# Optimization experiments

Hardware: AMD Instinct MI355X
Metric: run time of the kernel (lower is better)

Reference implementation:

```python
import jax, jax.numpy as jnp
import numpy as np

B, H, S, D = 2, 12, 2048, 128
SCALE = D ** (-0.5)
LAMBDA_INIT = 0.8


def setup_inputs() -> dict:
    key = jax.random.key(0)
    ks = jax.random.split(key, 5)
    shp = (B, H, S, D)
    return {
        "q1": jax.random.normal(ks[0], shp, dtype=jnp.float32),
        "k1": jax.random.normal(ks[1], shp, dtype=jnp.float32),
        "v": jax.random.normal(ks[2], shp, dtype=jnp.float32),
        "q2": jax.random.normal(ks[3], shp, dtype=jnp.float32),
        "k2": jax.random.normal(ks[4], shp, dtype=jnp.float32),
        # learnable lambda parameter, stored in log space (lambda_init=0.8)
        "lambda_log": jnp.full((1,), np.log(LAMBDA_INIT), dtype=jnp.float32),
    }


def _causal_attn(q, k, v, causal_mask):
    # q,k,v: [B,H,S,D]; causal_mask: [S,S] bool (True = keep)
    scores = jnp.einsum("bhqd,bhkd->bhqk", q, k) * SCALE
    neg = jnp.asarray(jnp.finfo(scores.dtype).min, scores.dtype)
    scores = jnp.where(causal_mask, scores, neg)
    weights = jax.nn.softmax(scores, axis=-1)
    return jnp.einsum("bhqk,bhkd->bhqd", weights, v)


def reference(q1, k1, v, q2, k2, lambda_log):
    seq = q1.shape[2]
    causal_mask = jnp.tril(jnp.ones((seq, seq), dtype=bool))
    attn1 = _causal_attn(q1, k1, v, causal_mask)
    attn2 = _causal_attn(q2, k2, v, causal_mask)
    lambda_val = jnp.exp(lambda_log).astype(q1.dtype)  # scalar-shaped (1,)
    return attn1 - lambda_val * attn2
```

## Files before the change

### kernel.cpp

```cpp
#include <hip/hip_runtime.h>

#define S_LEN 2048
#define D_DIM 128
#define NBH   24
#define TELEM (NBH * S_LEN * D_DIM)
#define SC2  (0.08838834764831845f * 1.44269504088896f)
#define MFIX 20.0f

typedef __bf16 bf16x8 __attribute__((ext_vector_type(8)));
typedef float f32x4 __attribute__((ext_vector_type(4)));
union Frag { bf16x8 v; unsigned short h[8]; uint4 q; };

#define PSTR 40
#define BUFU 12288
#define SMEM_USH (2 * BUFU)

__device__ __forceinline__ unsigned short f2bf(float f) {
    union { float f; unsigned u; } x; x.f = f;
    unsigned r = x.u + 0x7fffu + ((x.u >> 16) & 1u);
    return (unsigned short)(r >> 16);
}
__device__ __forceinline__ unsigned pk2bf(float a, float b) {
    return (unsigned)f2bf(a) | ((unsigned)f2bf(b) << 16);
}

typedef __attribute__((address_space(1))) const unsigned int gu32;
typedef __attribute__((address_space(3))) unsigned int lu32;
__device__ __forceinline__ void g2l16(const unsigned short* g, unsigned short* l) {
    __builtin_amdgcn_global_load_lds((gu32*)g, (lu32*)l, 16, 0, 0);
}

#define KBLK (TELEM / (8 * 256))
__global__ __launch_bounds__(256) void conv_kv(
    const float* __restrict__ gk1, const float* __restrict__ gk2, const float* __restrict__ gv,
    unsigned short* __restrict__ ok1, unsigned short* __restrict__ ok2,
    unsigned short* __restrict__ ovt)
{
    __shared__ __align__(16) unsigned short sT[128 * 40];
    const int b = blockIdx.x;
    if (b < 2 * KBLK) {
        const float* src = (b < KBLK) ? gk1 : gk2;
        unsigned short* dst = (b < KBLK) ? ok1 : ok2;
        const int bb = (b < KBLK) ? b : b - KBLK;
        const size_t base = ((size_t)bb * 256 + threadIdx.x) * 8;
        float4 a = *(const float4*)(src + base);
        float4 c = *(const float4*)(src + base + 4);
        uint4 w = {pk2bf(a.x, a.y), pk2bf(a.z, a.w), pk2bf(c.x, c.y), pk2bf(c.z, c.w)};
        *(uint4*)(dst + base) = w;
        return;
    }
    const int bx  = b - 2 * KBLK;
    const int tid  = threadIdx.x;
    const int wave = tid >> 6;
    const int lane = tid & 63;
    const int quad = lane >> 4;
    const int l16  = lane & 15;
    const int bh = bx >> 6;
    const int s0 = (bx & 63) * 32;
    const float* pv = gv + (size_t)bh * S_LEN * D_DIM + (size_t)s0 * D_DIM;
    const int vd0 = (wave >> 1) * 64 + l16 * 4;
    const int pq  = ((quad & 1) << 1) | (quad >> 1);
    #pragma unroll
    for (int i = 0; i < 4; ++i) {
        const int kvb = i * 8 + (wave & 1) * 4;
        float4 f = *(const float4*)(pv + (kvb + quad) * D_DIM + vd0);
        unsigned h01 = pk2bf(f.x, f.y), h23 = pk2bf(f.z, f.w);
        unsigned t01 = (unsigned)__shfl_xor((int)h01, 16);
        unsigned t23 = (unsigned)__shfl_xor((int)h23, 16);
        unsigned b01, b23;
        if (quad & 1) {
            b01 = (t23 & 0xffffu) | (h23 << 16);
            b23 = (t23 >> 16) | (h23 & 0xffff0000u);
        } else {
            b01 = (h01 & 0xffffu) | (t01 << 16);
            b23 = (h01 >> 16) | (t01 & 0xffff0000u);
        }
        unsigned s01 = (unsigned)__shfl_xor((int)b01, 32);
        unsigned s23 = (unsigned)__shfl_xor((int)b23, 32);
        uint2 w;
        if (quad & 2) { w.x = s23; w.y = b23; }
        else          { w.x = b01; w.y = s01; }
        *(uint2*)&sT[(vd0 + pq) * 40 + kvb] = w;
    }
    __syncthreads();
    const int d = tid >> 1;
    const int h = tid & 1;
    uint4 w0 = *(const uint4*)&sT[d * 40 + h * 16];
    uint4 w1 = *(const uint4*)&sT[d * 40 + h * 16 + 8];
    unsigned short* out = ovt + ((size_t)bh * D_DIM + d) * S_LEN + s0 + h * 16;
    *(uint4*)(out) = w0;
    *(uint4*)(out + 8) = w1;
}

__device__ __forceinline__ void stage_tile(
    unsigned short* smem, int boff, int w,
    const int* koff, const int* voff,
    const unsigned short* k1pl, const unsigned short* k2pl, const unsigned short* vpl,
    int kv0)
{
    const unsigned short* kp1 = k1pl + (size_t)kv0 * 128;
    const unsigned short* kp2 = k2pl + (size_t)kv0 * 128;
    const unsigned short* vp  = vpl + kv0;
    unsigned short* dk1 = smem + boff + w * 1024;
    unsigned short* dk2 = smem + boff + 4096 + w * 1024;
    unsigned short* dv  = smem + boff + 8192 + w * 1024;
    #pragma unroll
    for (int j = 0; j < 2; ++j) {
        g2l16(kp1 + koff[j], dk1 + j * 512);
        g2l16(kp2 + koff[j], dk2 + j * 512);
        g2l16(vp  + voff[j], dv  + j * 512);
    }
}

__global__ __launch_bounds__(256, 3) void diff_attn_fast(
    const float* __restrict__ gq1, const float* __restrict__ gq2,
    const float* __restrict__ gll,
    const unsigned short* __restrict__ k1b, const unsigned short* __restrict__ k2b,
    const unsigned short* __restrict__ vtb, float* __restrict__ gout)
{
    __shared__ __align__(16) unsigned short smem[SMEM_USH];

    const int tid  = threadIdx.x;
    const int w    = tid >> 6;
    const int lane = tid & 63;
    const int quad = lane >> 4;
    const int l16  = lane & 15;
    const int g    = w & 1;

    const int bid   = blockIdx.x;
    const int j     = bid / NBH;
    const int bh    = bid - j * NBH;
    const int i     = 31 - j;
    const int T     = 2 * i + 2;
    const int sidx  = (w < 2) ? (2 * i + 1) : (2 * i);
    const int qw    = sidx * 32;
    const int mytiles = sidx + 1;
    const size_t hoff = (size_t)bh * (S_LEN * D_DIM);

    const float lam = __expf(gll[0]);

    Frag q1f[4], q2f[4];
    {
        const float* p1 = gq1 + hoff + (size_t)(qw + g * 16 + l16) * D_DIM;
        const float* p2 = gq2 + hoff + (size_t)(qw + g * 16 + l16) * D_DIM;
        #pragma unroll
        for (int ks = 0; ks < 4; ++ks) {
            const int d0 = ks * 32 + quad * 8;
            float4 a = *(const float4*)(p1 + d0);
            float4 b = *(const float4*)(p1 + d0 + 4);
            q1f[ks].q = (uint4){pk2bf(a.x, a.y), pk2bf(a.z, a.w),
                                pk2bf(b.x, b.y), pk2bf(b.z, b.w)};
            a = *(const float4*)(p2 + d0);
            b = *(const float4*)(p2 + d0 + 4);
            q2f[ks].q = (uint4){pk2bf(a.x, a.y), pk2bf(a.z, a.w),
                                pk2bf(b.x, b.y), pk2bf(b.z, b.w)};
        }
    }

    int koff[2], voff[2];
    #pragma unroll
    for (int jj = 0; jj < 2; ++jj) {
        const int s = w * 8 + jj * 4 + quad;
        koff[jj] = s * 128 + ((l16 ^ (s & 15)) << 3);
        const int d = w * 32 + jj * 16 + (lane >> 2);
        voff[jj] = d * 2048 + (((lane & 3) ^ ((d >> 1) & 3)) << 3);
    }
    const unsigned short* k1pl = k1b + hoff;
    const unsigned short* k2pl = k2b + hoff;
    const unsigned short* vpl  = vtb + hoff;

    f32x4 o1[8], o2[8];
    #pragma unroll
    for (int ii = 0; ii < 8; ++ii) {
        o1[ii] = (f32x4){0.f, 0.f, 0.f, 0.f};
        o2[ii] = (f32x4){0.f, 0.f, 0.f, 0.f};
    }
    float l1a = 0.f, l2a = 0.f;

    __asm__ __volatile__("s_waitcnt vmcnt(0)" ::: "memory");
    stage_tile(smem, 0, w, koff, voff, k1pl, k2pl, vpl, 0);

    int boff = 0;
    for (int t = 0; t < T; ++t) {
        const int nboff = boff ^ BUFU;
        __asm__ __volatile__("s_waitcnt vmcnt(0) lgkmcnt(0)" ::: "memory");
        __builtin_amdgcn_s_barrier();
        __asm__ __volatile__("" ::: "memory");
        if (t + 1 < T)
            stage_tile(smem, nboff, w, koff, voff, k1pl, k2pl, vpl, (t + 1) * 32);

        if (t < mytiles) {
            const unsigned short* sK1 = smem + boff;
            const unsigned short* sK2 = smem + boff + 4096;
            const unsigned short* sVt = smem + boff + 8192;
            const int kv0 = t * 32;

            f32x4 sA[2], sB[2];
            #pragma unroll
            for (int sub = 0; sub < 2; ++sub) {
                sA[sub] = (f32x4){0.f, 0.f, 0.f, 0.f};
                sB[sub] = (f32x4){0.f, 0.f, 0.f, 0.f};
            }
            __builtin_amdgcn_s_setprio(1);
            #pragma unroll
            for (int sub = 0; sub < 2; ++sub) {
                const int srow = (sub * 16 + l16) * 128;
                #pragma unroll
                for (int ks = 0; ks < 4; ++ks) {
                    const int c = ks * 4 + quad;
                    Frag kf;
                    kf.q = *(const uint4*)&sK1[srow + ((c ^ l16) << 3)];
                    sA[sub] = __builtin_amdgcn_mfma_f32_16x16x32_bf16(kf.v, q1f[ks].v, sA[sub], 0, 0, 0);
                    kf.q = *(const uint4*)&sK2[srow + ((c ^ l16) << 3)];
                    sB[sub] = __builtin_amdgcn_mfma_f32_16x16x32_bf16(kf.v, q2f[ks].v, sB[sub], 0, 0, 0);
                }
            }
            __builtin_amdgcn_s_setprio(0);

            const bool full = (t < sidx);
            float p1v[8], p2v[8];
            if (full) {
                #pragma unroll
                for (int sub = 0; sub < 2; ++sub)
                    #pragma unroll
                    for (int r = 0; r < 4; ++r) {
                        p1v[sub * 4 + r] = __builtin_amdgcn_exp2f(sA[sub][r] * SC2 - MFIX);
                        p2v[sub * 4 + r] = __builtin_amdgcn_exp2f(sB[sub][r] * SC2 - MFIX);
                    }
            } else {
                const int qv = qw + g * 16 + l16;
                #pragma unroll
                for (int sub = 0; sub < 2; ++sub)
                    #pragma unroll
                    for (int r = 0; r < 4; ++r) {
                        const int kv = kv0 + sub * 16 + quad * 4 + r;
                        const bool ok = (kv <= qv);
                        p1v[sub * 4 + r] = __builtin_amdgcn_exp2f(ok ? sA[sub][r] * SC2 - MFIX : -1e30f);
                        p2v[sub * 4 + r] = __builtin_amdgcn_exp2f(ok ? sB[sub][r] * SC2 - MFIX : -1e30f);
                    }
            }
            float a1 = 0.f, a2 = 0.f;
            #pragma unroll
            for (int ii = 0; ii < 8; ++ii) { a1 += p1v[ii]; a2 += p2v[ii]; }
            l1a += a1; l2a += a2;

            Frag pf1, pf2;
            {
                unsigned a0 = pk2bf(p1v[0], p1v[1]);
                unsigned a1w = pk2bf(p1v[2], p1v[3]);
                unsigned a2 = pk2bf(p1v[4], p1v[5]);
                unsigned a3 = pk2bf(p1v[6], p1v[7]);
                asm("v_permlane32_swap_b32 %0, %1" : "+v"(a0), "+v"(a2));
                asm("v_permlane32_swap_b32 %0, %1" : "+v"(a1w), "+v"(a3));
                asm("v_permlane16_swap_b32 %0, %1" : "+v"(a0), "+v"(a2));
                asm("v_permlane16_swap_b32 %0, %1" : "+v"(a1w), "+v"(a3));
                pf1.q = (uint4){a0, a1w, a2, a3};
                unsigned b0 = pk2bf(p2v[0], p2v[1]);
                unsigned b1w = pk2bf(p2v[2], p2v[3]);
                unsigned b2 = pk2bf(p2v[4], p2v[5]);
                unsigned b3 = pk2bf(p2v[6], p2v[7]);
                asm("v_permlane32_swap_b32 %0, %1" : "+v"(b0), "+v"(b2));
                asm("v_permlane32_swap_b32 %0, %1" : "+v"(b1w), "+v"(b3));
                asm("v_permlane16_swap_b32 %0, %1" : "+v"(b0), "+v"(b2));
                asm("v_permlane16_swap_b32 %0, %1" : "+v"(b1w), "+v"(b3));
                pf2.q = (uint4){b0, b1w, b2, b3};
            }

            __builtin_amdgcn_s_setprio(1);
            #pragma unroll
            for (int cb = 0; cb < 8; ++cb) {
                const int d = cb * 16 + l16;
                Frag vf;
                vf.q = *(const uint4*)&sVt[d * 32 + ((quad ^ ((d >> 1) & 3)) << 3)];
                o1[cb] = __builtin_amdgcn_mfma_f32_16x16x32_bf16(vf.v, pf1.v, o1[cb], 0, 0, 0);
                o2[cb] = __builtin_amdgcn_mfma_f32_16x16x32_bf16(vf.v, pf2.v, o2[cb], 0, 0, 0);
            }
            __builtin_amdgcn_s_setprio(0);
        }
        boff = nboff;
    }

    __asm__ __volatile__("s_waitcnt lgkmcnt(0)" ::: "memory");
    __builtin_amdgcn_s_barrier();
    __asm__ __volatile__("" ::: "memory");

    float l1 = l1a, l2 = l2a;
    l1 += __shfl_xor(l1, 16); l1 += __shfl_xor(l1, 32);
    l2 += __shfl_xor(l2, 16); l2 += __shfl_xor(l2, 32);
    const float inv1 = 1.0f / l1;
    const float inv2 = lam / l2;
    float* sO = (float*)smem + w * 2112;
    #pragma unroll
    for (int cb = 0; cb < 8; ++cb) {
        f32x4 r = o1[cb] * inv1 - o2[cb] * inv2;
        *(f32x4*)&sO[l16 * 132 + cb * 16 + quad * 4] = r;
    }
    __asm__ __volatile__("s_waitcnt lgkmcnt(0)" ::: "memory");
    #pragma unroll
    for (int u = 0; u < 8; ++u) {
        const int row = u * 2 + (lane >> 5);
        const int d4  = lane & 31;
        f32x4 vv = *(const f32x4*)&sO[row * 132 + d4 * 4];
        *(f32x4*)(gout + hoff + (size_t)(qw + g * 16 + row) * D_DIM + d4 * 4) = vv;
    }
}

#define KSTR 136
#define VSTR2 40
#define foK1 0
#define foK2 (32 * KSTR)
#define foVt (2 * 32 * KSTR)
#define foP  (2 * 32 * KSTR + 128 * VSTR2)
#define FSMEM (foP + 4 * 2 * 16 * PSTR)

__global__ __launch_bounds__(256) void diff_attn_slow(
    const float* __restrict__ gq1, const float* __restrict__ gk1,
    const float* __restrict__ gv,  const float* __restrict__ gq2,
    const float* __restrict__ gk2, const float* __restrict__ gll,
    float* __restrict__ gout)
{
    __shared__ __align__(16) unsigned short smem[FSMEM];
    unsigned short* sK1 = smem + foK1;
    unsigned short* sK2 = smem + foK2;
    unsigned short* sVt = smem + foVt;

    const int tid  = threadIdx.x;
    const int wave = tid >> 6;
    const int lane = tid & 63;
    const int quad = lane >> 4;
    const int l16  = lane & 15;
    const int qb   = (int)gridDim.x - 1 - (int)blockIdx.x;
    const int bh   = blockIdx.y;
    const size_t hoff = (size_t)bh * S_LEN * D_DIM;
    const int qbase = qb * 64 + wave * 16;

    unsigned short* sP1 = smem + foP + (wave * 2 + 0) * 16 * PSTR;
    unsigned short* sP2 = smem + foP + (wave * 2 + 1) * 16 * PSTR;

    const float lam = __expf(gll[0]);

    Frag q1f[4], q2f[4];
    {
        const float* p1 = gq1 + hoff + (size_t)(qbase + l16) * D_DIM;
        const float* p2 = gq2 + hoff + (size_t)(qbase + l16) * D_DIM;
        #pragma unroll
        for (int ks = 0; ks < 4; ++ks) {
            const int d0 = ks * 32 + quad * 8;
            float4 a = *(const float4*)(p1 + d0);
            float4 b = *(const float4*)(p1 + d0 + 4);
            q1f[ks].q = (uint4){pk2bf(a.x, a.y), pk2bf(a.z, a.w),
                               pk2bf(b.x, b.y), pk2bf(b.z, b.w)};
            a = *(const float4*)(p2 + d0);
            b = *(const float4*)(p2 + d0 + 4);
            q2f[ks].q = (uint4){pk2bf(a.x, a.y), pk2bf(a.z, a.w),
                               pk2bf(b.x, b.y), pk2bf(b.z, b.w)};
        }
    }

    f32x4 o1[8], o2[8];
    #pragma unroll
    for (int i = 0; i < 8; ++i) {
        o1[i] = (f32x4){0.f, 0.f, 0.f, 0.f};
        o2[i] = (f32x4){0.f, 0.f, 0.f, 0.f};
    }
    float m1 = -1e30f, m2 = -1e30f, l1 = 0.f, l2 = 0.f;

    const int ntiles  = qb * 2 + 2;
    const int mytiles = (qbase + 15) / 32 + 1;

    const int vd0 = (wave >> 1) * 64 + l16 * 4;
    const int pq  = ((quad & 1) << 1) | (quad >> 1);

    for (int t = 0; t < ntiles; ++t) {
        __syncthreads();
        const int kv0 = t * 32;
        {
            const float* pk1 = gk1 + hoff + (size_t)kv0 * D_DIM;
            const float* pk2 = gk2 + hoff + (size_t)kv0 * D_DIM;
            #pragma unroll
            for (int i = 0; i < 4; ++i) {
                const int e   = i * 256 + tid;
                const int row = e >> 5;
                const int c4  = e & 31;
                const int go  = row * D_DIM + c4 * 4;
                float4 f = *(const float4*)(pk1 + go);
                uint2 w; w.x = pk2bf(f.x, f.y); w.y = pk2bf(f.z, f.w);
                *(uint2*)&sK1[row * KSTR + c4 * 4] = w;
                f = *(const float4*)(pk2 + go);
                w.x = pk2bf(f.x, f.y); w.y = pk2bf(f.z, f.w);
                *(uint2*)&sK2[row * KSTR + c4 * 4] = w;
            }
        }
        {
            const float* pv = gv + hoff + (size_t)kv0 * D_DIM;
            #pragma unroll
            for (int i = 0; i < 4; ++i) {
                const int kvb = i * 8 + (wave & 1) * 4;
                float4 f = *(const float4*)(pv + (kvb + quad) * D_DIM + vd0);
                unsigned h01 = pk2bf(f.x, f.y), h23 = pk2bf(f.z, f.w);
                unsigned t01 = (unsigned)__shfl_xor((int)h01, 16);
                unsigned t23 = (unsigned)__shfl_xor((int)h23, 16);
                unsigned b01, b23;
                if (quad & 1) {
                    b01 = (t23 & 0xffffu) | (h23 << 16);
                    b23 = (t23 >> 16) | (h23 & 0xffff0000u);
                } else {
                    b01 = (h01 & 0xffffu) | (t01 << 16);
                    b23 = (h01 >> 16) | (t01 & 0xffff0000u);
                }
                unsigned s01 = (unsigned)__shfl_xor((int)b01, 32);
                unsigned s23 = (unsigned)__shfl_xor((int)b23, 32);
                uint2 w;
                if (quad & 2) { w.x = s23; w.y = b23; }
                else          { w.x = b01; w.y = s01; }
                *(uint2*)&sVt[(vd0 + pq) * VSTR2 + kvb] = w;
            }
        }
        __syncthreads();
        if (t >= mytiles) continue;

        f32x4 s1[2], s2[2];
        #pragma unroll
        for (int sub = 0; sub < 2; ++sub) {
            s1[sub] = (f32x4){0.f, 0.f, 0.f, 0.f};
            s2[sub] = (f32x4){0.f, 0.f, 0.f, 0.f};
            const int ro = (sub * 16 + l16) * KSTR + quad * 8;
            #pragma unroll
            for (int ks = 0; ks < 4; ++ks) {
                Frag kf;
                kf.q = *(const uint4*)&sK1[ro + ks * 32];
                s1[sub] = __builtin_amdgcn_mfma_f32_16x16x32_bf16(kf.v, q1f[ks].v, s1[sub], 0, 0, 0);
                kf.q = *(const uint4*)&sK2[ro + ks * 32];
                s2[sub] = __builtin_amdgcn_mfma_f32_16x16x32_bf16(kf.v, q2f[ks].v, s2[sub], 0, 0, 0);
            }
        }

        const int qv = qbase + l16;
        {
            float a[8];
            #pragma unroll
            for (int sub = 0; sub < 2; ++sub)
                #pragma unroll
                for (int r = 0; r < 4; ++r) {
                    const int kv = kv0 + sub * 16 + quad * 4 + r;
                    a[sub * 4 + r] = (kv <= qv) ? s1[sub][r] * SC2 : -__builtin_inff();
                }
            float mt = a[0];
            #pragma unroll
            for (int i = 1; i < 8; ++i) mt = fmaxf(mt, a[i]);
            mt = fmaxf(mt, __shfl_xor(mt, 16));
            mt = fmaxf(mt, __shfl_xor(mt, 32));
            const float mn = fmaxf(m1, mt);
            const float al = __builtin_amdgcn_exp2f(m1 - mn);
            m1 = mn;
            float p[8], rs = 0.f;
            #pragma unroll
            for (int i = 0; i < 8; ++i) { p[i] = __builtin_amdgcn_exp2f(a[i] - mn); rs += p[i]; }
            rs += __shfl_xor(rs, 16);
            rs += __shfl_xor(rs, 32);
            l1 = l1 * al + rs;
            #pragma unroll
            for (int cb = 0; cb < 8; ++cb) o1[cb] *= al;
            uint2 w;
            w.x = pk2bf(p[0], p[1]); w.y = pk2bf(p[2], p[3]);
            *(uint2*)&sP1[l16 * PSTR + quad * 4] = w;
            w.x = pk2bf(p[4], p[5]); w.y = pk2bf(p[6], p[7]);
            *(uint2*)&sP1[l16 * PSTR + 16 + quad * 4] = w;
        }
        {
            float a[8];
            #pragma unroll
            for (int sub = 0; sub < 2; ++sub)
                #pragma unroll
                for (int r = 0; r < 4; ++r) {
                    const int kv = kv0 + sub * 16 + quad * 4 + r;
                    a[sub * 4 + r] = (kv <= qv) ? s2[sub][r] * SC2 : -__builtin_inff();
                }
            float mt = a[0];
            #pragma unroll
            for (int i = 1; i < 8; ++i) mt = fmaxf(mt, a[i]);
            mt = fmaxf(mt, __shfl_xor(mt, 16));
            mt = fmaxf(mt, __shfl_xor(mt, 32));
            const float mn = fmaxf(m2, mt);
            const float al = __builtin_amdgcn_exp2f(m2 - mn);
            m2 = mn;
            float p[8], rs = 0.f;
            #pragma unroll
            for (int i = 0; i < 8; ++i) { p[i] = __builtin_amdgcn_exp2f(a[i] - mn); rs += p[i]; }
            rs += __shfl_xor(rs, 16);
            rs += __shfl_xor(rs, 32);
            l2 = l2 * al + rs;
            #pragma unroll
            for (int cb = 0; cb < 8; ++cb) o2[cb] *= al;
            uint2 w;
            w.x = pk2bf(p[0], p[1]); w.y = pk2bf(p[2], p[3]);
            *(uint2*)&sP2[l16 * PSTR + quad * 4] = w;
            w.x = pk2bf(p[4], p[5]); w.y = pk2bf(p[6], p[7]);
            *(uint2*)&sP2[l16 * PSTR + 16 + quad * 4] = w;
        }

        __asm__ __volatile__("s_waitcnt lgkmcnt(0)" ::: "memory");

        Frag pf1, pf2;
        pf1.q = *(const uint4*)&sP1[l16 * PSTR + quad * 8];
        pf2.q = *(const uint4*)&sP2[l16 * PSTR + quad * 8];
        #pragma unroll
        for (int cb = 0; cb < 8; ++cb) {
            Frag vf;
            vf.q = *(const uint4*)&sVt[(cb * 16 + l16) * VSTR2 + quad * 8];
            o1[cb] = __builtin_amdgcn_mfma_f32_16x16x32_bf16(vf.v, pf1.v, o1[cb], 0, 0, 0);
            o2[cb] = __builtin_amdgcn_mfma_f32_16x16x32_bf16(vf.v, pf2.v, o2[cb], 0, 0, 0);
        }
    }

    __syncthreads();
    float* sO = (float*)smem + wave * (16 * 132);
    const float inv1 = 1.0f / l1;
    const float inv2 = lam / l2;
    #pragma unroll
    for (int cb = 0; cb < 8; ++cb) {
        f32x4 r = o1[cb] * inv1 - o2[cb] * inv2;
        *(f32x4*)&sO[l16 * 132 + cb * 16 + quad * 4] = r;
    }
    __asm__ __volatile__("s_waitcnt lgkmcnt(0)" ::: "memory");
    #pragma unroll
    for (int u = 0; u < 8; ++u) {
        const int row = u * 2 + (lane >> 5);
        const int d4  = lane & 31;
        f32x4 vv = *(const f32x4*)&sO[row * 132 + d4 * 4];
        *(f32x4*)(gout + hoff + (size_t)(qbase + row) * D_DIM + d4 * 4) = vv;
    }
}

extern "C" void kernel_launch(void* const* d_in, const int* in_sizes, int n_in,
                              void* d_out, int out_size, void* d_ws, size_t ws_size,
                              hipStream_t stream) {
    (void)in_sizes; (void)n_in; (void)out_size;
    const float* gq1 = (const float*)d_in[0];
    const float* gk1 = (const float*)d_in[1];
    const float* gv  = (const float*)d_in[2];
    const float* gq2 = (const float*)d_in[3];
    const float* gk2 = (const float*)d_in[4];
    const float* gll = (const float*)d_in[5];
    float* gout = (float*)d_out;

    const size_t need = (size_t)3 * TELEM * sizeof(unsigned short);
    if (ws_size >= need) {
        unsigned short* k1b = (unsigned short*)d_ws;
        unsigned short* k2b = k1b + TELEM;
        unsigned short* vtb = k2b + TELEM;
        hipLaunchKernelGGL(conv_kv, dim3(2 * KBLK + NBH * (S_LEN / 32)), dim3(256), 0, stream,
                           gk1, gk2, gv, k1b, k2b, vtb);
        hipLaunchKernelGGL(diff_attn_fast, dim3(32 * NBH), dim3(256), 0, stream,
                           gq1, gq2, gll, k1b, k2b, vtb, gout);
    } else {
        hipLaunchKernelGGL(diff_attn_slow, dim3(S_LEN / 64, NBH), dim3(256), 0, stream,
                           gq1, gk1, gv, gq2, gk2, gll, gout);
    }
}
```

Before: 237.1 us.

## Rebalance causal work by splitting late KV tiles between waves per branch

Each block now pairs a short query tile (pairi) with a long one (63-pairi). All waves first process the shared prefix of KV tiles. After that, the waves that own the short tile write their output and reload q2 for the long tile, so for the remaining tiles one wave pair computes branch 1 and the other computes branch 2. Partial o2 and l2 are then merged through LDS. The aim is to stop waves idling at the barriers on the causal tail, at the cost of an extra q reload and an LDS reduction. Output stores now go straight from registers to global memory instead of being staged through LDS for coalescing.

```diff
diff --git a/kernel.cpp b/kernel.cpp
--- a/kernel.cpp
+++ b/kernel.cpp
@@ -22,6 +22,22 @@
 }
 __device__ __forceinline__ unsigned pk2bf(float a, float b) {
     return (unsigned)f2bf(a) | ((unsigned)f2bf(b) << 16);
+}
+__device__ __forceinline__ float wred(float x) {
+    x += __shfl_xor(x, 16);
+    x += __shfl_xor(x, 32);
+    return x;
+}
+__device__ __forceinline__ void butterfly(const float* p, Frag& pf) {
+    unsigned a0 = pk2bf(p[0], p[1]);
+    unsigned a1 = pk2bf(p[2], p[3]);
+    unsigned a2 = pk2bf(p[4], p[5]);
+    unsigned a3 = pk2bf(p[6], p[7]);
+    asm("v_permlane32_swap_b32 %0, %1" : "+v"(a0), "+v"(a2));
+    asm("v_permlane32_swap_b32 %0, %1" : "+v"(a1), "+v"(a3));
+    asm("v_permlane16_swap_b32 %0, %1" : "+v"(a0), "+v"(a2));
+    asm("v_permlane16_swap_b32 %0, %1" : "+v"(a1), "+v"(a3));
+    pf.q = (uint4){a0, a1, a2, a3};
 }
 
 typedef __attribute__((address_space(1))) const unsigned int gu32;
@@ -112,6 +128,60 @@
     }
 }
 
+__device__ __forceinline__ void half_body(
+    int l16, int quad, int t, int qv2, bool full,
+    const Frag (&qf)[4], f32x4 (&o)[8], float& la,
+    const unsigned short* sK, const unsigned short* sVt)
+{
+    f32x4 s[2];
+    s[0] = (f32x4){0.f, 0.f, 0.f, 0.f};
+    s[1] = (f32x4){0.f, 0.f, 0.f, 0.f};
+    __builtin_amdgcn_s_setprio(1);
+    #pragma unroll
+    for (int sub = 0; sub < 2; ++sub) {
+        const int srow = (sub * 16 + l16) * 128;
+        #pragma unroll
+        for (int ks = 0; ks < 4; ++ks) {
+            const int c = ks * 4 + quad;
+            Frag kf;
+            kf.q = *(const uint4*)&sK[srow + ((c ^ l16) << 3)];
+            s[sub] = __builtin_amdgcn_mfma_f32_16x16x32_bf16(kf.v, qf[ks].v, s[sub], 0, 0, 0);
+        }
+    }
+    __builtin_amdgcn_s_setprio(0);
+    float p[8];
+    if (full) {
+        #pragma unroll
+        for (int sub = 0; sub < 2; ++sub)
+            #pragma unroll
+            for (int r = 0; r < 4; ++r)
+                p[sub * 4 + r] = __builtin_amdgcn_exp2f(s[sub][r] * SC2 - MFIX);
+    } else {
+        #pragma unroll
+        for (int sub = 0; sub < 2; ++sub)
+            #pragma unroll
+            for (int r = 0; r < 4; ++r) {
+                const int kv = t * 32 + sub * 16 + quad * 4 + r;
+                p[sub * 4 + r] = __builtin_amdgcn_exp2f((kv <= qv2) ? s[sub][r] * SC2 - MFIX : -1e30f);
+            }
+    }
+    float a = 0.f;
+    #pragma unroll
+    for (int i = 0; i < 8; ++i) a += p[i];
+    la += a;
+    Frag pf;
+    butterfly(p, pf);
+    __builtin_amdgcn_s_setprio(1);
+    #pragma unroll
+    for (int cb = 0; cb < 8; ++cb) {
+        const int d = cb * 16 + l16;
+        Frag vf;
+        vf.q = *(const uint4*)&sVt[d * 32 + ((quad ^ ((d >> 1) & 3)) << 3)];
+        o[cb] = __builtin_amdgcn_mfma_f32_16x16x32_bf16(vf.v, pf.v, o[cb], 0, 0, 0);
+    }
+    __builtin_amdgcn_s_setprio(0);
+}
+
 __global__ __launch_bounds__(256, 3) void diff_attn_fast(
     const float* __restrict__ gq1, const float* __restrict__ gq2,
     const float* __restrict__ gll,
@@ -128,13 +198,11 @@
     const int g    = w & 1;
 
     const int bid   = blockIdx.x;
-    const int j     = bid / NBH;
-    const int bh    = bid - j * NBH;
-    const int i     = 31 - j;
-    const int T     = 2 * i + 2;
-    const int sidx  = (w < 2) ? (2 * i + 1) : (2 * i);
-    const int qw    = sidx * 32;
-    const int mytiles = sidx + 1;
+    const int pairi = bid / NBH;
+    const int bh    = bid - pairi * NBH;
+    const int sAi   = 63 - pairi;
+    const int T     = 64 - pairi;
+    const int qw    = (w < 2) ? sAi * 32 : pairi * 32;
     const size_t hoff = (size_t)bh * (S_LEN * D_DIM);
 
     const float lam = __expf(gll[0]);
@@ -181,127 +249,157 @@
     stage_tile(smem, 0, w, koff, voff, k1pl, k2pl, vpl, 0);
 
     int boff = 0;
-    for (int t = 0; t < T; ++t) {
-        const int nboff = boff ^ BUFU;
+    const int qv = qw + g * 16 + l16;
+    for (int t = 0; t <= pairi; ++t) {
         __asm__ __volatile__("s_waitcnt vmcnt(0) lgkmcnt(0)" ::: "memory");
         __builtin_amdgcn_s_barrier();
         __asm__ __volatile__("" ::: "memory");
         if (t + 1 < T)
-            stage_tile(smem, nboff, w, koff, voff, k1pl, k2pl, vpl, (t + 1) * 32);
-
-        if (t < mytiles) {
-            const unsigned short* sK1 = smem + boff;
-            const unsigned short* sK2 = smem + boff + 4096;
-            const unsigned short* sVt = smem + boff + 8192;
-            const int kv0 = t * 32;
-
-            f32x4 sA[2], sB[2];
-            #pragma unroll
-            for (int sub = 0; sub < 2; ++sub) {
-                sA[sub] = (f32x4){0.f, 0.f, 0.f, 0.f};
-                sB[sub] = (f32x4){0.f, 0.f, 0.f, 0.f};
+            stage_tile(smem, boff ^ BUFU, w, koff, voff, k1pl, k2pl, vpl, (t + 1) * 32);
+
+        const unsigned short* sK1 = smem + boff;
+        const unsigned short* sK2 = smem + boff + 4096;
+        const unsigned short* sVt = smem + boff + 8192;
+        const int kv0 = t * 32;
+
+        f32x4 sA[2], sB[2];
+        #pragma unroll
+        for (int sub = 0; sub < 2; ++sub) {
+            sA[sub] = (f32x4){0.f, 0.f, 0.f, 0.f};
+            sB[sub] = (f32x4){0.f, 0.f, 0.f, 0.f};
+        }
+        __builtin_amdgcn_s_setprio(1);
+        #pragma unroll
+        for (int sub = 0; sub < 2; ++sub) {
+            const int srow = (sub * 16 + l16) * 128;
+            #pragma unroll
+            for (int ks = 0; ks < 4; ++ks) {
+                const int c = ks * 4 + quad;
+                Frag kf;
+                kf.q = *(const uint4*)&sK1[srow + ((c ^ l16) << 3)];
+                sA[sub] = __builtin_amdgcn_mfma_f32_16x16x32_bf16(kf.v, q1f[ks].v, sA[sub], 0, 0, 0);
+                kf.q = *(const uint4*)&sK2[srow + ((c ^ l16) << 3)];
+                sB[sub] = __builtin_amdgcn_mfma_f32_16x16x32_bf16(kf.v, q2f[ks].v, sB[sub], 0, 0, 0);
             }
-            __builtin_amdgcn_s_setprio(1);
-            #pragma unroll
-            for (int sub = 0; sub < 2; ++sub) {
-                const int srow = (sub * 16 + l16) * 128;
+        }
+        __builtin_amdgcn_s_setprio(0);
+
+        const bool full = (w < 2) || (t < pairi);
+        float p1v[8], p2v[8];
+        if (full) {
+            #pragma unroll
+            for (int sub = 0; sub < 2; ++sub)
                 #pragma unroll
-                for (int ks = 0; ks < 4; ++ks) {
-                    const int c = ks * 4 + quad;
-                    Frag kf;
-                    kf.q = *(const uint4*)&sK1[srow + ((c ^ l16) << 3)];
-                    sA[sub] = __builtin_amdgcn_mfma_f32_16x16x32_bf16(kf.v, q1f[ks].v, sA[sub], 0, 0, 0);
-                    kf.q = *(const uint4*)&sK2[srow + ((c ^ l16) << 3)];
-                    sB[sub] = __builtin_amdgcn_mfma_f32_16x16x32_bf16(kf.v, q2f[ks].v, sB[sub], 0, 0, 0);
+                for (int r = 0; r < 4; ++r) {
+                    p1v[sub * 4 + r] = __builtin_amdgcn_exp2f(sA[sub][r] * SC2 - MFIX);
+                    p2v[sub * 4 + r] = __builtin_amdgcn_exp2f(sB[sub][r] * SC2 - MFIX);
                 }
-            }
-            __builtin_amdgcn_s_setprio(0);
-
-            const bool full = (t < sidx);
-            float p1v[8], p2v[8];
-            if (full) {
+        } else {
+            #pragma unroll
+            for (int sub = 0; sub < 2; ++sub)
                 #pragma unroll
-                for (int sub = 0; sub < 2; ++sub)
-                    #pragma unroll
-                    for (int r = 0; r < 4; ++r) {
-                        p1v[sub * 4 + r] = __builtin_amdgcn_exp2f(sA[sub][r] * SC2 - MFIX);
-                        p2v[sub * 4 + r] = __builtin_amdgcn_exp2f(sB[sub][r] * SC2 - MFIX);
-                    }
-            } else {
-                const int qv = qw + g * 16 + l16;
-                #pragma unroll
-                for (int sub = 0; sub < 2; ++sub)
-                    #pragma unroll
-                    for (int r = 0; r < 4; ++r) {
-                        const int kv = kv0 + sub * 16 + quad * 4 + r;
-                        const bool ok = (kv <= qv);
-                        p1v[sub * 4 + r] = __builtin_amdgcn_exp2f(ok ? sA[sub][r] * SC2 - MFIX : -1e30f);
-                        p2v[sub * 4 + r] = __builtin_amdgcn_exp2f(ok ? sB[sub][r] * SC2 - MFIX : -1e30f);
-                    }
-            }
-            float a1 = 0.f, a2 = 0.f;
-            #pragma unroll
-            for (int ii = 0; ii < 8; ++ii) { a1 += p1v[ii]; a2 += p2v[ii]; }
-            l1a += a1; l2a += a2;
-
-            Frag pf1, pf2;
-            {
-                unsigned a0 = pk2bf(p1v[0], p1v[1]);
-                unsigned a1w = pk2bf(p1v[2], p1v[3]);
-                unsigned a2 = pk2bf(p1v[4], p1v[5]);
-                unsigned a3 = pk2bf(p1v[6], p1v[7]);
-                asm("v_permlane32_swap_b32 %0, %1" : "+v"(a0), "+v"(a2));
-                asm("v_permlane32_swap_b32 %0, %1" : "+v"(a1w), "+v"(a3));
-                asm("v_permlane16_swap_b32 %0, %1" : "+v"(a0), "+v"(a2));
-                asm("v_permlane16_swap_b32 %0, %1" : "+v"(a1w), "+v"(a3));
-                pf1.q = (uint4){a0, a1w, a2, a3};
-                unsigned b0 = pk2bf(p2v[0], p2v[1]);
-                unsigned b1w = pk2bf(p2v[2], p2v[3]);
-                unsigned b2 = pk2bf(p2v[4], p2v[5]);
-                unsigned b3 = pk2bf(p2v[6], p2v[7]);
-                asm("v_permlane32_swap_b32 %0, %1" : "+v"(b0), "+v"(b2));
-                asm("v_permlane32_swap_b32 %0, %1" : "+v"(b1w), "+v"(b3));
-                asm("v_permlane16_swap_b32 %0, %1" : "+v"(b0), "+v"(b2));
-                asm("v_permlane16_swap_b32 %0, %1" : "+v"(b1w), "+v"(b3));
-                pf2.q = (uint4){b0, b1w, b2, b3};
-            }
-
-            __builtin_amdgcn_s_setprio(1);
-            #pragma unroll
-            for (int cb = 0; cb < 8; ++cb) {
-                const int d = cb * 16 + l16;
-                Frag vf;
-                vf.q = *(const uint4*)&sVt[d * 32 + ((quad ^ ((d >> 1) & 3)) << 3)];
-                o1[cb] = __builtin_amdgcn_mfma_f32_16x16x32_bf16(vf.v, pf1.v, o1[cb], 0, 0, 0);
-                o2[cb] = __builtin_amdgcn_mfma_f32_16x16x32_bf16(vf.v, pf2.v, o2[cb], 0, 0, 0);
-            }
-            __builtin_amdgcn_s_setprio(0);
-        }
-        boff = nboff;
+                for (int r = 0; r < 4; ++r) {
+                    const int kv = kv0 + sub * 16 + quad * 4 + r;
+                    const bool ok = (kv <= qv);
+                    p1v[sub * 4 + r] = __builtin_amdgcn_exp2f(ok ? sA[sub][r] * SC2 - MFIX : -1e30f);
+                    p2v[sub * 4 + r] = __builtin_amdgcn_exp2f(ok ? sB[sub][r] * SC2 - MFIX : -1e30f);
+                }
+        }
+        float a1 = 0.f, a2 = 0.f;
+        #pragma unroll
+        for (int ii = 0; ii < 8; ++ii) { a1 += p1v[ii]; a2 += p2v[ii]; }
+        l1a += a1; l2a += a2;
+
+        Frag pf1, pf2;
+        butterfly(p1v, pf1);
+        butterfly(p2v, pf2);
+
+        __builtin_amdgcn_s_setprio(1);
+        #pragma unroll
+        for (int cb = 0; cb < 8; ++cb) {
+            const int d = cb * 16 + l16;
+            Frag vf;
+            vf.q = *(const uint4*)&sVt[d * 32 + ((quad ^ ((d >> 1) & 3)) << 3)];
+            o1[cb] = __builtin_amdgcn_mfma_f32_16x16x32_bf16(vf.v, pf1.v, o1[cb], 0, 0, 0);
+            o2[cb] = __builtin_amdgcn_mfma_f32_16x16x32_bf16(vf.v, pf2.v, o2[cb], 0, 0, 0);
+        }
+        __builtin_amdgcn_s_setprio(0);
+        boff ^= BUFU;
+    }
+
+    if (w >= 2) {
+        const float l1 = wred(l1a);
+        const float l2 = wred(l2a);
+        const float inv1 = 1.0f / l1;
+        const float inv2 = lam / l2;
+        float* outp = gout + hoff + (size_t)(qw + g * 16 + l16) * D_DIM + quad * 4;
+        #pragma unroll
+        for (int cb = 0; cb < 8; ++cb) {
+            f32x4 r = o1[cb] * inv1 - o2[cb] * inv2;
+            *(f32x4*)(outp + cb * 16) = r;
+        }
+        const float* p2 = gq2 + hoff + (size_t)(sAi * 32 + g * 16 + l16) * D_DIM;
+        #pragma unroll
+        for (int ks = 0; ks < 4; ++ks) {
+            const int d0 = ks * 32 + quad * 8;
+            float4 a = *(const float4*)(p2 + d0);
+            float4 b = *(const float4*)(p2 + d0 + 4);
+            q2f[ks].q = (uint4){pk2bf(a.x, a.y), pk2bf(a.z, a.w),
+                                pk2bf(b.x, b.y), pk2bf(b.z, b.w)};
+        }
+        #pragma unroll
+        for (int ii = 0; ii < 8; ++ii) o2[ii] = (f32x4){0.f, 0.f, 0.f, 0.f};
+        l2a = 0.f;
+    }
+
+    const int qv2 = sAi * 32 + g * 16 + l16;
+    for (int t = pairi + 1; t < T; ++t) {
+        __asm__ __volatile__("s_waitcnt vmcnt(0) lgkmcnt(0)" ::: "memory");
+        __builtin_amdgcn_s_barrier();
+        __asm__ __volatile__("" ::: "memory");
+        if (t + 1 < T)
+            stage_tile(smem, boff ^ BUFU, w, koff, voff, k1pl, k2pl, vpl, (t + 1) * 32);
+
+        const unsigned short* sVt = smem + boff + 8192;
+        const bool full = (t < sAi);
+        if (w < 2)
+            half_body(l16, quad, t, qv2, full, q1f, o1, l1a, smem + boff, sVt);
+        else
+            half_body(l16, quad, t, qv2, full, q2f, o2, l2a, smem + boff + 4096, sVt);
+        boff ^= BUFU;
     }
 
     __asm__ __volatile__("s_waitcnt lgkmcnt(0)" ::: "memory");
     __builtin_amdgcn_s_barrier();
     __asm__ __volatile__("" ::: "memory");
-
-    float l1 = l1a, l2 = l2a;
-    l1 += __shfl_xor(l1, 16); l1 += __shfl_xor(l1, 32);
-    l2 += __shfl_xor(l2, 16); l2 += __shfl_xor(l2, 32);
-    const float inv1 = 1.0f / l1;
-    const float inv2 = lam / l2;
-    float* sO = (float*)smem + w * 2112;
-    #pragma unroll
-    for (int cb = 0; cb < 8; ++cb) {
-        f32x4 r = o1[cb] * inv1 - o2[cb] * inv2;
-        *(f32x4*)&sO[l16 * 132 + cb * 16 + quad * 4] = r;
+    if (w >= 2) {
+        float* dst = (float*)smem + g * 2368;
+        const int base = lane * 37;
+        #pragma unroll
+        for (int cb = 0; cb < 8; ++cb)
+            *(f32x4*)&dst[base + cb * 4] = o2[cb];
+        dst[base + 32] = l2a;
     }
     __asm__ __volatile__("s_waitcnt lgkmcnt(0)" ::: "memory");
-    #pragma unroll
-    for (int u = 0; u < 8; ++u) {
-        const int row = u * 2 + (lane >> 5);
-        const int d4  = lane & 31;
-        f32x4 vv = *(const f32x4*)&sO[row * 132 + d4 * 4];
-        *(f32x4*)(gout + hoff + (size_t)(qw + g * 16 + row) * D_DIM + d4 * 4) = vv;
+    __builtin_amdgcn_s_barrier();
+    __asm__ __volatile__("" ::: "memory");
+    if (w < 2) {
+        const float* src = (const float*)smem + g * 2368;
+        const int base = lane * 37;
+        #pragma unroll
+        for (int cb = 0; cb < 8; ++cb)
+            o2[cb] += *(const f32x4*)&src[base + cb * 4];
+        l2a += src[base + 32];
+        const float l1 = wred(l1a);
+        const float l2 = wred(l2a);
+        const float inv1 = 1.0f / l1;
+        const float inv2 = lam / l2;
+        float* outp = gout + hoff + (size_t)(qw + g * 16 + l16) * D_DIM + quad * 4;
+        #pragma unroll
+        for (int cb = 0; cb < 8; ++cb) {
+            f32x4 r = o1[cb] * inv1 - o2[cb] * inv2;
+            *(f32x4*)(outp + cb * 16) = r;
+        }
     }
 }
 
```

Result: faster. 231.6 us (-2.4%).
